# Kernel tuning notes

Measured on AMD Instinct MI355X. Metric: run time of the kernel, lower is better.

Reference implementation:

```python
import jax, jax.numpy as jnp
import numpy as np

NUM_Z = 100   # atomic-number bins hardcoded in the module
G = 512       # number of graphs in the batch (segment count)


def setup_inputs() -> dict:
    key = jax.random.key(0)
    k1, k2, k3 = jax.random.split(key, 3)
    N, D = 50000, 64
    out = jax.random.normal(k1, (N, D), dtype=jnp.float32)
    # atomic numbers in [1, 100], matching the (z-1)*D offset logic
    z_rv = jax.random.randint(k2, (N,), 1, NUM_Z + 1)
    # sorted graph ids in [0, G)
    x_rv_batch = jnp.sort(jax.random.randint(k3, (N,), 0, G))
    return {"out": out, "z_rv": z_rv, "x_rv_batch": x_rv_batch}


def reference(out, z_rv, x_rv_batch):
    # Original math: elem_pool[i, (z_i-1)*D : z_i*D] = out[i] (zeros elsewhere),
    # then global_mean_pool(elem_pool, batch) -> [G, 100*D].
    # Fused form: segment-sum node features into (graph, atomic-number) bins,
    # then divide by per-graph node counts. Identical result, no NxD*100 buffer.
    N, D = out.shape
    keys = x_rv_batch * NUM_Z + (z_rv - 1)                 # [N] combined (graph, bin) id
    sums = jax.ops.segment_sum(out, keys, num_segments=G * NUM_Z)   # [G*100, D]
    counts = jax.ops.segment_sum(jnp.ones((N,), out.dtype), x_rv_batch,
                                 num_segments=G)           # [G] nodes per graph
    pooled = sums.reshape(G, NUM_Z * D) / jnp.maximum(counts, 1.0)[:, None]
    return pooled
```

## Files before the change

### kernel.cpp

```cpp
#include <hip/hip_runtime.h>

#define NUM_Z 100
#define NUM_G 512
#define DIM   64
#define THREADS 1024
#define CHUNK 1024

__device__ __forceinline__ int lower_bound_wave(const int* __restrict__ arr, int n,
                                                int target, int lane) {
    int lo = 0, len = n;
    while (len > 0) {
        int step = (len + 63) >> 6;
        int idx  = lo + lane * step;
        int v    = (idx < n) ? arr[idx] : 0x7fffffff;
        unsigned long long m = __ballot(v < target);
        int k = (int)__popcll(m);
        if (k == 0) break;
        int rem = k * step; if (rem > len) rem = len;
        int hi  = lo + rem;
        lo += (k - 1) * step + 1;
        len = hi - lo;
    }
    return lo;
}

__global__ __launch_bounds__(THREADS) void anp_sort_kernel(
    const float4* __restrict__ feat,
    const int*    __restrict__ z,
    const int*    __restrict__ batch,
    float*        __restrict__ pooled,
    int n)
{
    __shared__ int hist[128];
    __shared__ int scan_tmp[128];
    __shared__ int pref[NUM_Z + 1];
    __shared__ int cursor[NUM_Z];
    __shared__ unsigned short idx_sorted[CHUNK];
    __shared__ int sb[2];
    __shared__ int wtot;

    const int g    = blockIdx.x;
    const int tid  = threadIdx.x;
    const int wave = tid >> 6;
    const int lane = tid & 63;
    const int grp  = tid >> 4;
    const int q    = tid & 15;
    const int b0   = 2 * grp;

    if (wave < 2) {
        int r = lower_bound_wave(batch, n, g + wave, lane);
        if (lane == 0) sb[wave] = r;
    }
    __syncthreads();
    const int start = sb[0];
    const int end   = sb[1];
    const int cnt   = end - start;

    float4 a0 = make_float4(0.f, 0.f, 0.f, 0.f);
    float4 a1 = make_float4(0.f, 0.f, 0.f, 0.f);

    for (int cs = start; cs < end; cs += CHUNK) {
        const int m = min(CHUNK, end - cs);

        if (tid < 128) hist[tid] = 0;
        __syncthreads();

        int zv = 0;
        if (tid < m) {
            zv = z[cs + tid] - 1;
            atomicAdd(&hist[zv], 1);
        }
        __syncthreads();

        if (wave < 2) {
            int e = hist[(wave << 6) + lane];
            #pragma unroll
            for (int d = 1; d < 64; d <<= 1) {
                int t = __shfl_up(e, d, 64);
                if (lane >= d) e += t;
            }
            scan_tmp[(wave << 6) + lane] = e;
            if (wave == 0 && lane == 63) wtot = e;
        }
        __syncthreads();

        if (tid <= NUM_Z) {
            int v = (tid == 0) ? 0
                  : scan_tmp[tid - 1] + ((tid - 1) >= 64 ? wtot : 0);
            pref[tid] = v;
            if (tid < NUM_Z) cursor[tid] = v;
        }
        __syncthreads();

        if (tid < m) {
            int p = atomicAdd(&cursor[zv], 1);
            idx_sorted[p] = (unsigned short)(tid | ((zv & 1) << 15));
        }
        __syncthreads();

        if (grp < 50) {
            const int off = pref[b0];
            const int c   = pref[b0 + 2] - off;
            for (int base = 0; base < c; base += 16) {
                const int nb = min(16, c - base);
                int myraw = (q < nb) ? (int)idx_sorted[off + base + q] : 0;
                #pragma unroll 4
                for (int j = 0; j < nb; ++j) {
                    int raw  = __shfl(myraw, ((lane >> 4) << 4) + j, 64);
                    int nd   = raw & 0x7fff;
                    float pm = (float)(raw >> 15);
                    float4 v = feat[(size_t)(cs + nd) * 16 + q];
                    float m0 = 1.0f - pm;
                    a0.x = fmaf(v.x, m0, a0.x); a0.y = fmaf(v.y, m0, a0.y);
                    a0.z = fmaf(v.z, m0, a0.z); a0.w = fmaf(v.w, m0, a0.w);
                    a1.x = fmaf(v.x, pm, a1.x); a1.y = fmaf(v.y, pm, a1.y);
                    a1.z = fmaf(v.z, pm, a1.z); a1.w = fmaf(v.w, pm, a1.w);
                }
            }
        }
        __syncthreads();
    }

    if (grp < 50) {
        const float s = 1.0f / (float)(cnt > 1 ? cnt : 1);
        float4* outv = (float4*)(pooled + (size_t)g * (NUM_Z * DIM));
        outv[(b0 + 0) * 16 + q] = make_float4(a0.x*s, a0.y*s, a0.z*s, a0.w*s);
        outv[(b0 + 1) * 16 + q] = make_float4(a1.x*s, a1.y*s, a1.z*s, a1.w*s);
    }
}

extern "C" void kernel_launch(void* const* d_in, const int* in_sizes, int n_in,
                              void* d_out, int out_size, void* d_ws, size_t ws_size,
                              hipStream_t stream) {
    const float* feat  = (const float*)d_in[0];
    const int*   z     = (const int*)d_in[1];
    const int*   batch = (const int*)d_in[2];
    float* pooled = (float*)d_out;
    const int n = in_sizes[0] / DIM;

    anp_sort_kernel<<<NUM_G, THREADS, 0, stream>>>(
        (const float4*)feat, z, batch, pooled, n);
}
```

Before: 12.15 us.

## Split each graph across four blocks of 256 threads by bin slices

Each graph now runs on four 256-thread blocks, and each block owns 25 of the 100 atomic-number bins. Every block still histograms and counting-sorts the graph's nodes in chunks of 256, but gathers features only for its own bin slice. The bin-parity mask is XORed with the slice parity so that odd-offset slices still map nodes to the right accumulator. The aim is more blocks and better occupancy across CUs instead of 512 large blocks. The cost is that the sort and histogram work is repeated four times, and graphs of about 100 nodes may need more than one chunk pass.

```diff
diff --git a/kernel.cpp b/kernel.cpp
--- a/kernel.cpp
+++ b/kernel.cpp
@@ -3,8 +3,10 @@
 #define NUM_Z 100
 #define NUM_G 512
 #define DIM   64
-#define THREADS 1024
-#define CHUNK 1024
+#define BPG   4
+#define BINS_PB 25
+#define THREADS 256
+#define CHUNK 256
 
 __device__ __forceinline__ int lower_bound_wave(const int* __restrict__ arr, int n,
                                                 int target, int lane) {
@@ -24,7 +26,7 @@
     return lo;
 }
 
-__global__ __launch_bounds__(THREADS) void anp_sort_kernel(
+__global__ __launch_bounds__(THREADS) void anp_split_kernel(
     const float4* __restrict__ feat,
     const int*    __restrict__ z,
     const int*    __restrict__ batch,
@@ -39,14 +41,16 @@
     __shared__ int sb[2];
     __shared__ int wtot;
 
-    const int g    = blockIdx.x;
-    const int tid  = threadIdx.x;
-    const int wave = tid >> 6;
-    const int lane = tid & 63;
-    const int grp  = tid >> 4;
-    const int q    = tid & 15;
-    const int b0   = 2 * grp;
+    const int g     = blockIdx.x >> 2;
+    const int slice = blockIdx.x & 3;
+    const int tid   = threadIdx.x;
+    const int wave  = tid >> 6;
+    const int lane  = tid & 63;
+    const int grp   = tid >> 4;
+    const int q     = tid & 15;
+    const int sp    = slice & 1;
 
+    if (tid < 128) hist[tid] = 0;
     if (wave < 2) {
         int r = lower_bound_wave(batch, n, g + wave, lane);
         if (lane == 0) sb[wave] = r;
@@ -61,9 +65,6 @@
 
     for (int cs = start; cs < end; cs += CHUNK) {
         const int m = min(CHUNK, end - cs);
-
-        if (tid < 128) hist[tid] = 0;
-        __syncthreads();
 
         int zv = 0;
         if (tid < m) {
@@ -98,9 +99,11 @@
         }
         __syncthreads();
 
-        if (grp < 50) {
-            const int off = pref[b0];
-            const int c   = pref[b0 + 2] - off;
+        if (grp < 13) {
+            const int gb0 = slice * BINS_PB + 2 * grp;
+            const int gbe = slice * BINS_PB + min(2 * grp + 2, BINS_PB);
+            const int off = pref[gb0];
+            const int c   = pref[gbe] - off;
             for (int base = 0; base < c; base += 16) {
                 const int nb = min(16, c - base);
                 int myraw = (q < nb) ? (int)idx_sorted[off + base + q] : 0;
@@ -108,24 +111,30 @@
                 for (int j = 0; j < nb; ++j) {
                     int raw  = __shfl(myraw, ((lane >> 4) << 4) + j, 64);
                     int nd   = raw & 0x7fff;
-                    float pm = (float)(raw >> 15);
+                    float m1 = (float)((raw >> 15) ^ sp);
                     float4 v = feat[(size_t)(cs + nd) * 16 + q];
-                    float m0 = 1.0f - pm;
+                    float m0 = 1.0f - m1;
                     a0.x = fmaf(v.x, m0, a0.x); a0.y = fmaf(v.y, m0, a0.y);
                     a0.z = fmaf(v.z, m0, a0.z); a0.w = fmaf(v.w, m0, a0.w);
-                    a1.x = fmaf(v.x, pm, a1.x); a1.y = fmaf(v.y, pm, a1.y);
-                    a1.z = fmaf(v.z, pm, a1.z); a1.w = fmaf(v.w, pm, a1.w);
+                    a1.x = fmaf(v.x, m1, a1.x); a1.y = fmaf(v.y, m1, a1.y);
+                    a1.z = fmaf(v.z, m1, a1.z); a1.w = fmaf(v.w, m1, a1.w);
                 }
             }
         }
-        __syncthreads();
+        if (cs + CHUNK < end) {
+            __syncthreads();
+            if (tid < 128) hist[tid] = 0;
+            __syncthreads();
+        }
     }
 
-    if (grp < 50) {
+    if (grp < 13) {
         const float s = 1.0f / (float)(cnt > 1 ? cnt : 1);
         float4* outv = (float4*)(pooled + (size_t)g * (NUM_Z * DIM));
-        outv[(b0 + 0) * 16 + q] = make_float4(a0.x*s, a0.y*s, a0.z*s, a0.w*s);
-        outv[(b0 + 1) * 16 + q] = make_float4(a1.x*s, a1.y*s, a1.z*s, a1.w*s);
+        const int gb0 = slice * BINS_PB + 2 * grp;
+        outv[gb0 * 16 + q] = make_float4(a0.x*s, a0.y*s, a0.z*s, a0.w*s);
+        if (2 * grp + 1 < BINS_PB)
+            outv[(gb0 + 1) * 16 + q] = make_float4(a1.x*s, a1.y*s, a1.z*s, a1.w*s);
     }
 }
 
@@ -138,6 +147,6 @@
     float* pooled = (float*)d_out;
     const int n = in_sizes[0] / DIM;
 
-    anp_sort_kernel<<<NUM_G, THREADS, 0, stream>>>(
+    anp_split_kernel<<<NUM_G * BPG, THREADS, 0, stream>>>(
         (const float4*)feat, z, batch, pooled, n);
 }
```

Result: slower. 12.54 us (+3.2%).
